# Kernel optimization log

Hardware: AMD Instinct MI355X
Metric: run time of the kernel (lower is better)

## Reference

```python
import jax, jax.numpy as jnp
import numpy as np

EPS = 1e-6
H = 16

def setup_inputs() -> dict:
    key = jax.random.key(0)
    ks = jax.random.split(key, 11)
    B, L, D = 4, 4096, 1024
    sc = 1.0 / np.sqrt(D)
    return {
        "queries": jax.random.normal(ks[0], (B, L, D), jnp.float32),
        "keys": jax.random.normal(ks[1], (B, L, D), jnp.float32),
        "values": jax.random.normal(ks[2], (B, L, D), jnp.float32),
        "Wq": jax.random.normal(ks[3], (D, D), jnp.float32) * sc,
        "bq": jax.random.normal(ks[4], (D,), jnp.float32) * 0.01,
        "Wk": jax.random.normal(ks[5], (D, D), jnp.float32) * sc,
        "bk": jax.random.normal(ks[6], (D,), jnp.float32) * 0.01,
        "Wv": jax.random.normal(ks[7], (D, D), jnp.float32) * sc,
        "bv": jax.random.normal(ks[8], (D,), jnp.float32) * 0.01,
        "Wo": jax.random.normal(ks[9], (D, D), jnp.float32) * sc,
        "bo": jax.random.normal(ks[10], (D,), jnp.float32) * 0.01,
    }

def reference(queries, keys, values, Wq, bq, Wk, bk, Wv, bv, Wo, bo):
    B, L, _ = queries.shape
    S = keys.shape[1]
    # projections + split heads: [B, H, L, dh]
    q = (queries @ Wq + bq).reshape(B, L, H, -1).transpose(0, 2, 1, 3)
    k = (keys @ Wk + bk).reshape(B, S, H, -1).transpose(0, 2, 1, 3)
    v = (values @ Wv + bv).reshape(B, S, H, -1).transpose(0, 2, 1, 3)
    # kernel feature map
    q = jax.nn.sigmoid(q)
    k = jax.nn.sigmoid(k)
    # flow normalization (sink/source)
    sink_incoming = 1.0 / jnp.einsum('nhld,nhd->nhl', q + EPS, k.sum(axis=2) + EPS)
    source_outgoing = 1.0 / jnp.einsum('nhld,nhd->nhl', k + EPS, q.sum(axis=2) + EPS)
    conserved_sink = jnp.einsum('nhld,nhd->nhl', q + EPS,
                                (k * source_outgoing[..., None]).sum(axis=2) + EPS)
    conserved_source = jnp.einsum('nhld,nhd->nhl', k + EPS,
                                  (q * sink_incoming[..., None]).sum(axis=2) + EPS)
    conserved_source = jnp.clip(conserved_source, -1.0, 1.0)
    sink_allocation = jax.nn.sigmoid(conserved_sink * (float(L) / float(S)))
    source_competition = jax.nn.softmax(conserved_source, axis=-1) * float(S)
    # linear attention: kv then q(kv)
    qn = q * sink_incoming[..., None]
    vn = v * source_competition[..., None]
    kv = jnp.einsum('nhld,nhlm->nhdm', k, vn)
    x = jnp.einsum('nhld,nhdm->nhlm', qn, kv) * sink_allocation[..., None]
    x = x.transpose(0, 2, 1, 3).reshape(B, L, -1)
    return x @ Wo + bo
```

## Files before the change

kernel.cpp:

```cpp
#include <hip/hip_runtime.h>

#define Bc 4
#define Lc 4096
#define Dc 1024
#define LDQ 3072
#define Mc (Bc*Lc)
#define EPSc 1e-6f

typedef __bf16 bf16x8 __attribute__((ext_vector_type(8)));
typedef __bf16 bf16x4 __attribute__((ext_vector_type(4)));
typedef float f32x4 __attribute__((ext_vector_type(4)));

typedef __attribute__((address_space(3))) void lds_vt;
typedef const __attribute__((address_space(1))) void gbl_vt;

__device__ __forceinline__ void gll16(const void* g, void* l) {
  __builtin_amdgcn_global_load_lds((gbl_vt*)g, (lds_vt*)l, 16, 0, 0);
}

__global__ __launch_bounds__(256) void conv3(const float* __restrict__ Q, const float* __restrict__ K,
                                             const float* __restrict__ V, __bf16* __restrict__ Y) {
  const float* src = (blockIdx.y == 0) ? Q : (blockIdx.y == 1) ? K : V;
  __bf16* dst = Y + (size_t)blockIdx.y * ((size_t)Mc * Dc);
  const int i = blockIdx.x * 256 + threadIdx.x;
  const float4 v = ((const float4*)src)[i];
  bf16x4 o;
  o[0] = (__bf16)v.x; o[1] = (__bf16)v.y; o[2] = (__bf16)v.z; o[3] = (__bf16)v.w;
  ((bf16x4*)dst)[i] = o;
}

__global__ __launch_bounds__(256) void wt_conv4(const float* __restrict__ W0, const float* __restrict__ W1,
                                                const float* __restrict__ W2, const float* __restrict__ W3,
                                                __bf16* __restrict__ T) {
  const float* W = (blockIdx.z == 0) ? W0 : (blockIdx.z == 1) ? W1 : (blockIdx.z == 2) ? W2 : W3;
  __bf16* Wt = T + (size_t)blockIdx.z * ((size_t)Dc * Dc);
  __shared__ float t[32][33];
  const int n0 = blockIdx.x << 5, k0 = blockIdx.y << 5;
  const int tx = threadIdx.x, ty = threadIdx.y;
#pragma unroll
  for (int i = 0; i < 4; ++i)
    t[ty + 8 * i][tx] = W[(size_t)(k0 + ty + 8 * i) * Dc + n0 + tx];
  __syncthreads();
#pragma unroll
  for (int i = 0; i < 4; ++i)
    Wt[(size_t)(n0 + ty + 8 * i) * Dc + k0 + tx] = (__bf16)t[tx][ty + 8 * i];
}

template <int FUSED>
__global__ __launch_bounds__(256, 4) void gemm128b(
    const __bf16* __restrict__ Aq_, const __bf16* __restrict__ Ak_, const __bf16* __restrict__ Av_,
    const __bf16* __restrict__ Wq_, const __bf16* __restrict__ Wk_, const __bf16* __restrict__ Wv_,
    const float* __restrict__ bq_, const float* __restrict__ bk_, const float* __restrict__ bv_,
    void* __restrict__ Cp, float* __restrict__ qsum, float* __restrict__ ksum) {
  __shared__ __bf16 As[2][128 * 32];
  __shared__ __bf16 Bs[2][128 * 32];
  const int tid = threadIdx.x;
  const int lane = tid & 63, w4 = tid >> 6;
  const int wr = w4 >> 1, wc = w4 & 1;
  const int lf = lane & 15, kq = lane >> 4;

  constexpr int NCT = FUSED ? 24 : 8;
  constexpr int CPX = (128 * NCT) >> 3;
  const int hwlin = blockIdx.x + (blockIdx.y << 7);
  const int swz = (hwlin & 7) * CPX + (hwlin >> 3);
  const int bx = swz / NCT, ct = swz - bx * NCT;
  const int row0 = bx << 7, col0 = ct << 7;
  const int region = FUSED ? (ct >> 3) : 0;
  const int colL = FUSED ? (col0 & 1023) : col0;

  const __bf16* Agl = FUSED ? (region == 0 ? Aq_ : (region == 1 ? Ak_ : Av_)) : Aq_;
  const __bf16* Bgl = FUSED ? (region == 0 ? Wq_ : (region == 1 ? Wk_ : Wv_)) : Wq_;
  const float* biasp = FUSED ? (region == 0 ? bq_ : (region == 1 ? bk_ : bv_)) : bq_;
  const __bf16* Ab_g = Agl + (size_t)row0 * 1024;
  const __bf16* Bb_g = Bgl + (size_t)colL * 1024;

  const int srow = (w4 << 5) + (lane >> 2);
  const int sgd = lane & 3;
  const int ssrc = (sgd ^ ((lane >> 3) & 3)) << 3;
  const size_t aoff0 = (size_t)srow * 1024 + ssrc;
  const size_t aoff1 = (size_t)(srow + 16) * 1024 + ssrc;
  const int ldst0 = srow * 32 + (sgd << 3);
  const int ldst1 = (srow + 16) * 32 + (sgd << 3);

  const int kgsw = (kq ^ ((lf >> 1) & 3)) << 3;
  const int arb = (wr * 64 + lf) * 32 + kgsw;
  const int brb = (wc * 64 + lf) * 32 + kgsw;

  f32x4 acc[4][4] = {};

  for (int t = 0; t < 16; ++t) {
    const int kb = t << 6;
    gll16(Ab_g + aoff0 + kb, &As[0][ldst0]);
    gll16(Ab_g + aoff1 + kb, &As[0][ldst1]);
    gll16(Bb_g + aoff0 + kb, &Bs[0][ldst0]);
    gll16(Bb_g + aoff1 + kb, &Bs[0][ldst1]);
    gll16(Ab_g + aoff0 + kb + 32, &As[1][ldst0]);
    gll16(Ab_g + aoff1 + kb + 32, &As[1][ldst1]);
    gll16(Bb_g + aoff0 + kb + 32, &Bs[1][ldst0]);
    gll16(Bb_g + aoff1 + kb + 32, &Bs[1][ldst1]);
    __syncthreads();
#pragma unroll
    for (int hf = 0; hf < 2; ++hf) {
      bf16x8 af[4], bfr[4];
#pragma unroll
      for (int m = 0; m < 4; ++m) af[m] = *(const bf16x8*)(&As[hf][0] + arb + m * 512);
#pragma unroll
      for (int n = 0; n < 4; ++n) bfr[n] = *(const bf16x8*)(&Bs[hf][0] + brb + n * 512);
#pragma unroll
      for (int m = 0; m < 4; ++m)
#pragma unroll
        for (int n = 0; n < 4; ++n)
          acc[m][n] = __builtin_amdgcn_mfma_f32_16x16x32_bf16(bfr[n], af[m], acc[m][n], 0, 0, 0);
    }
    __syncthreads();
  }

  const int b_of = row0 >> 12;
  const int orow = row0 + wr * 64 + lf;
  const int ocl = wc * 64 + (kq << 2);
#pragma unroll
  for (int n = 0; n < 4; ++n) {
    const int cl = ocl + (n << 4);
    const int cb = colL + cl;
    const f32x4 bb = *(const f32x4*)&biasp[cb];
    f32x4 sacc = {0.f, 0.f, 0.f, 0.f};
#pragma unroll
    for (int m = 0; m < 4; ++m) {
      f32x4 v = acc[m][n] + bb;
      if (FUSED && region < 2) {
#pragma unroll
        for (int r = 0; r < 4; ++r) v[r] = 1.0f / (1.0f + expf(-v[r]));
      }
      if (FUSED) {
        bf16x4 o;
#pragma unroll
        for (int r = 0; r < 4; ++r) o[r] = (__bf16)v[r];
        *(bf16x4*)&((__bf16*)Cp)[(size_t)(orow + (m << 4)) * LDQ + col0 + cl] = o;
      } else {
        *(f32x4*)&((float*)Cp)[(size_t)(orow + (m << 4)) * 1024 + col0 + cl] = v;
      }
      sacc += v;
    }
    if (FUSED && region < 2) {
#pragma unroll
      for (int o = 1; o < 16; o <<= 1) {
        sacc[0] += __shfl_xor(sacc[0], o); sacc[1] += __shfl_xor(sacc[1], o);
        sacc[2] += __shfl_xor(sacc[2], o); sacc[3] += __shfl_xor(sacc[3], o);
      }
      if (lf == 0) {
        float* sums = (region == 0) ? qsum : ksum;
#pragma unroll
        for (int r = 0; r < 4; ++r) atomicAdd(&sums[b_of * 1024 + cb + r], sacc[r]);
      }
    }
  }
}

template <int FUSED>
__global__ __launch_bounds__(256, 2) void gemm256x128(
    const __bf16* __restrict__ Aq_, const __bf16* __restrict__ Ak_, const __bf16* __restrict__ Av_,
    const __bf16* __restrict__ Wq_, const __bf16* __restrict__ Wk_, const __bf16* __restrict__ Wv_,
    const float* __restrict__ bq_, const float* __restrict__ bk_, const float* __restrict__ bv_,
    void* __restrict__ Cp, float* __restrict__ qsum, float* __restrict__ ksum) {
  __shared__ __bf16 As[256 * 32];
  __shared__ __bf16 Bs[128 * 32];
  const int tid = threadIdx.x;
  const int lane = tid & 63, w4 = tid >> 6;
  const int wr = w4 >> 1, wc = w4 & 1;
  const int lf = lane & 15, kq = lane >> 4;

  constexpr int NCT = FUSED ? 24 : 8;
  constexpr int CPX = (64 * NCT) >> 3;
  const int hwlin = blockIdx.x + blockIdx.y * 64;
  const int swz = (hwlin & 7) * CPX + (hwlin >> 3);
  const int bx = swz / NCT, ct = swz - bx * NCT;
  const int row0 = bx << 8, col0 = ct << 7;
  const int region = FUSED ? (ct >> 3) : 0;
  const int colL = FUSED ? (col0 & 1023) : col0;

  const __bf16* Agl = FUSED ? (region == 0 ? Aq_ : (region == 1 ? Ak_ : Av_)) : Aq_;
  const __bf16* Bgl = FUSED ? (region == 0 ? Wq_ : (region == 1 ? Wk_ : Wv_)) : Wq_;
  const float* biasp = FUSED ? (region == 0 ? bq_ : (region == 1 ? bk_ : bv_)) : bq_;
  const __bf16* Ab_g = Agl + (size_t)row0 * 1024;
  const __bf16* Bb_g = Bgl + (size_t)colL * 1024;

  int arow[4], asrc[4];
#pragma unroll
  for (int i = 0; i < 4; ++i) {
    const int g = i * 256 + tid;
    arow[i] = g >> 2;
    asrc[i] = ((g & 3) ^ ((arow[i] >> 1) & 3)) << 3;
  }
  const int kgsw = (kq ^ ((lf >> 1) & 3)) << 3;
  const int arb = (wr * 128 + lf) * 32 + kgsw;
  const int brb = (wc * 64 + lf) * 32 + kgsw;

  f32x4 acc[8][4] = {};

  for (int t = 0; t < 32; ++t) {
    const int kb = t << 5;
#pragma unroll
    for (int i = 0; i < 4; ++i)
      gll16(Ab_g + (size_t)arow[i] * 1024 + kb + asrc[i], &As[(i * 256 + tid) * 8]);
#pragma unroll
    for (int i = 0; i < 2; ++i)
      gll16(Bb_g + (size_t)arow[i] * 1024 + kb + asrc[i], &Bs[(i * 256 + tid) * 8]);
    __syncthreads();
    bf16x8 af[8], bfr[4];
#pragma unroll
    for (int m = 0; m < 8; ++m) af[m] = *(const bf16x8*)(As + arb + m * 512);
#pragma unroll
    for (int n = 0; n < 4; ++n) bfr[n] = *(const bf16x8*)(Bs + brb + n * 512);
#pragma unroll
    for (int m = 0; m < 8; ++m)
#pragma unroll
      for (int n = 0; n < 4; ++n)
        acc[m][n] = __builtin_amdgcn_mfma_f32_16x16x32_bf16(bfr[n], af[m], acc[m][n], 0, 0, 0);
    __syncthreads();
  }

  const int b_of = row0 >> 12;
  const int orow = row0 + wr * 128 + lf;
  const int ocl = wc * 64 + (kq << 2);
#pragma unroll
  for (int n = 0; n < 4; ++n) {
    const int cl = ocl + (n << 4);
    const int cb = colL + cl;
    const f32x4 bb = *(const f32x4*)&biasp[cb];
    f32x4 sacc = {0.f, 0.f, 0.f, 0.f};
#pragma unroll
    for (int m = 0; m < 8; ++m) {
      f32x4 v = acc[m][n] + bb;
      if (FUSED && region < 2) {
#pragma unroll
        for (int r = 0; r < 4; ++r) v[r] = 1.0f / (1.0f + expf(-v[r]));
      }
      if (FUSED) {
        bf16x4 o;
#pragma unroll
        for (int r = 0; r < 4; ++r) o[r] = (__bf16)v[r];
        *(bf16x4*)&((__bf16*)Cp)[(size_t)(orow + (m << 4)) * LDQ + col0 + cl] = o;
      } else {
        *(f32x4*)&((float*)Cp)[(size_t)(orow + (m << 4)) * 1024 + col0 + cl] = v;
      }
      sacc += v;
    }
    if (FUSED && region < 2) {
#pragma unroll
      for (int o = 1; o < 16; o <<= 1) {
        sacc[0] += __shfl_xor(sacc[0], o); sacc[1] += __shfl_xor(sacc[1], o);
        sacc[2] += __shfl_xor(sacc[2], o); sacc[3] += __shfl_xor(sacc[3], o);
      }
      if (lf == 0) {
        float* sums = (region == 0) ? qsum : ksum;
#pragma unroll
        for (int r = 0; r < 4; ++r) atomicAdd(&sums[b_of * 1024 + cb + r], sacc[r]);
      }
    }
  }
}

__global__ __launch_bounds__(256) void r2_flow(const __bf16* __restrict__ Qp, const __bf16* __restrict__ Kp,
                                               const float* __restrict__ ksum, const float* __restrict__ qsum,
                                               float* __restrict__ si,
                                               float* __restrict__ qsi, float* __restrict__ kso) {
  const int blk = blockIdx.x;
  const int chunk = blk & 15, bh = blk >> 4;
  const int b = bh >> 4, h = bh & 15;
  const int d = threadIdx.x & 63, w = threadIdx.x >> 6;
  __shared__ float ksE[64], qsE[64];
  if (threadIdx.x < 64) ksE[threadIdx.x] = ksum[bh * 64 + threadIdx.x] + EPSc;
  else if (threadIdx.x < 128) qsE[threadIdx.x - 64] = qsum[bh * 64 + threadIdx.x - 64] + EPSc;
  __syncthreads();
  const float kE = ksE[d], qE = qsE[d];
  const size_t base = ((size_t)b * Lc) * LDQ + h * 64 + d;
  const size_t obase = (size_t)bh * Lc;
  float qsia = 0.f, ksoa = 0.f;
  const int l0 = chunk * 256;
  for (int i = w; i < 256; i += 4) {
    const int l = l0 + i;
    const size_t idx = base + (size_t)l * LDQ;
    const float qv = (float)Qp[idx], kvv = (float)Kp[idx];
    float a = (qv + EPSc) * kE;
    float c2 = (kvv + EPSc) * qE;
#pragma unroll
    for (int o = 32; o; o >>= 1) { a += __shfl_xor(a, o); c2 += __shfl_xor(c2, o); }
    const float sil = 1.0f / a, sol = 1.0f / c2;
    if (d == 0) si[obase + l] = sil;
    qsia += qv * sil;
    ksoa += kvv * sol;
  }
  atomicAdd(&qsi[bh * 64 + d], qsia);
  atomicAdd(&kso[bh * 64 + d], ksoa);
}

__global__ __launch_bounds__(256) void r3_cons(const __bf16* __restrict__ Qp, const __bf16* __restrict__ Kp,
                                               const float* __restrict__ qsi, const float* __restrict__ kso,
                                               float* __restrict__ sa, float* __restrict__ csx,
                                               float* __restrict__ den) {
  const int blk = blockIdx.x;
  const int chunk = blk & 15, bh = blk >> 4;
  const int b = bh >> 4, h = bh & 15;
  const int d = threadIdx.x & 63, w = threadIdx.x >> 6;
  __shared__ float ksoE[64], qsiE[64];
  if (threadIdx.x < 64) ksoE[threadIdx.x] = kso[bh * 64 + threadIdx.x] + EPSc;
  else if (threadIdx.x < 128) qsiE[threadIdx.x - 64] = qsi[bh * 64 + threadIdx.x - 64] + EPSc;
  __syncthreads();
  const float kE = ksoE[d], qE = qsiE[d];
  const size_t base = ((size_t)b * Lc) * LDQ + h * 64 + d;
  const size_t obase = (size_t)bh * Lc;
  const int l0 = chunk * 256;
  float eacc = 0.f;
  for (int i = w; i < 256; i += 4) {
    const int l = l0 + i;
    const size_t idx = base + (size_t)l * LDQ;
    const float qv = (float)Qp[idx], kvv = (float)Kp[idx];
    float a = (qv + EPSc) * kE;
    float c2 = (kvv + EPSc) * qE;
#pragma unroll
    for (int o = 32; o; o >>= 1) { a += __shfl_xor(a, o); c2 += __shfl_xor(c2, o); }
    if (d == 0) {
      sa[obase + l] = 1.0f / (1.0f + expf(-a));
      const float cl = fminf(1.0f, fmaxf(-1.0f, c2));
      const float e = expf(cl);
      csx[obase + l] = e;
      eacc += e;
    }
  }
  if (d == 0) atomicAdd(&den[bh], eacc);
}

__global__ __launch_bounds__(256) void k5_kv(const __bf16* __restrict__ Kp, const __bf16* __restrict__ Vp,
                                             const float* __restrict__ csx, const float* __restrict__ den,
                                             float* __restrict__ kvout) {
  const int bh = blockIdx.x, chunk = blockIdx.y;
  const int b = bh >> 4, h = bh & 15;
  const int tid = threadIdx.x;
  const int dq = (tid >> 4) << 2;
  const int mq = (tid & 15) << 2;
  const float sden = 4096.0f / den[bh];
  __shared__ float klds[4][64], vlds[4][64];
  float acc[4][4] = {};
  const int r = tid >> 6, c = tid & 63;
  const size_t rowbase = ((size_t)b * Lc + chunk * 512) * LDQ + h * 64;
  const size_t csbase = (size_t)bh * Lc + chunk * 512;
  for (int i = 0; i < 512; i += 4) {
    const size_t idx = rowbase + (size_t)(i + r) * LDQ + c;
    const float sc = csx[csbase + i + r] * sden;
    klds[r][c] = (float)Kp[idx];
    vlds[r][c] = (float)Vp[idx] * sc;
    __syncthreads();
#pragma unroll
    for (int rr = 0; rr < 4; ++rr) {
      float kr[4], vr[4];
#pragma unroll
      for (int j = 0; j < 4; ++j) { kr[j] = klds[rr][dq + j]; vr[j] = vlds[rr][mq + j]; }
#pragma unroll
      for (int a = 0; a < 4; ++a)
#pragma unroll
        for (int e = 0; e < 4; ++e) acc[a][e] += kr[a] * vr[e];
    }
    __syncthreads();
  }
#pragma unroll
  for (int a = 0; a < 4; ++a)
#pragma unroll
    for (int e = 0; e < 4; ++e)
      atomicAdd(&kvout[(size_t)bh * 4096 + (dq + a) * 64 + mq + e], acc[a][e]);
}

__global__ __launch_bounds__(256) void k6_x(const __bf16* __restrict__ Qp,
                                            const float* __restrict__ kvin, const float* __restrict__ si,
                                            const float* __restrict__ sa, __bf16* __restrict__ Xb) {
  const int bh = blockIdx.x, chunk = blockIdx.y;
  const int b = bh >> 4, h = bh & 15;
  const int tid = threadIdx.x, lane = tid & 63, w = tid >> 6;
  const int lf = lane & 15, kq = lane >> 4;
  __shared__ float ktl[64][66];
  for (int e = tid; e < 4096; e += 256)
    ktl[e & 63][e >> 6] = kvin[(size_t)bh * 4096 + e];
  __syncthreads();
  bf16x8 kh[4][2], kl[4][2];
#pragma unroll
  for (int mi = 0; mi < 4; ++mi)
#pragma unroll
    for (int hf = 0; hf < 2; ++hf) {
      const float* p = &ktl[mi * 16 + lf][hf * 32 + kq * 8];
      bf16x8 hi, lo;
#pragma unroll
      for (int j = 0; j < 8; ++j) {
        const float f = p[j];
        hi[j] = (__bf16)f;
        lo[j] = (__bf16)(f - (float)hi[j]);
      }
      kh[mi][hf] = hi; kl[mi][hf] = lo;
    }
  const size_t bL = (size_t)b * Lc;
  const size_t obase = (size_t)bh * Lc;
#pragma unroll
  for (int gi = 0; gi < 4; ++gi) {
    const int lrow = chunk * 256 + (w * 4 + gi) * 16 + lf;
    const size_t qb = (bL + lrow) * LDQ + h * 64;
    const bf16x8 qf0 = *(const bf16x8*)(Qp + qb + kq * 8);
    const bf16x8 qf1 = *(const bf16x8*)(Qp + qb + 32 + kq * 8);
    const float sc = si[obase + lrow] * sa[obase + lrow];
    f32x4 acc[4] = {};
#pragma unroll
    for (int mi = 0; mi < 4; ++mi) {
      acc[mi] = __builtin_amdgcn_mfma_f32_16x16x32_bf16(kh[mi][0], qf0, acc[mi], 0, 0, 0);
      acc[mi] = __builtin_amdgcn_mfma_f32_16x16x32_bf16(kh[mi][1], qf1, acc[mi], 0, 0, 0);
      acc[mi] = __builtin_amdgcn_mfma_f32_16x16x32_bf16(kl[mi][0], qf0, acc[mi], 0, 0, 0);
      acc[mi] = __builtin_amdgcn_mfma_f32_16x16x32_bf16(kl[mi][1], qf1, acc[mi], 0, 0, 0);
    }
#pragma unroll
    for (int mi = 0; mi < 4; ++mi) {
      bf16x4 o;
#pragma unroll
      for (int r = 0; r < 4; ++r) o[r] = (__bf16)(acc[mi][r] * sc);
      *(bf16x4*)&Xb[(bL + lrow) * Dc + h * 64 + mi * 16 + (kq << 2)] = o;
    }
  }
}

extern "C" void kernel_launch(void* const* d_in, const int* in_sizes, int n_in,
                              void* d_out, int out_size, void* d_ws, size_t ws_size,
                              hipStream_t stream) {
  const float* Qin = (const float*)d_in[0];
  const float* Kin = (const float*)d_in[1];
  const float* Vin = (const float*)d_in[2];
  const float* Wq = (const float*)d_in[3];
  const float* bq = (const float*)d_in[4];
  const float* Wk = (const float*)d_in[5];
  const float* bk = (const float*)d_in[6];
  const float* Wv = (const float*)d_in[7];
  const float* bv = (const float*)d_in[8];
  const float* Wo = (const float*)d_in[9];
  const float* bo = (const float*)d_in[10];

  const size_t MD = (size_t)Mc * Dc;
  __bf16* Aq = (__bf16*)d_ws;
  __bf16* Ak = Aq + MD;
  __bf16* Av = Ak + MD;
  __bf16* Wqt = Av + MD;
  __bf16* Wkt = Wqt + (size_t)Dc * Dc;
  __bf16* Wvt = Wkt + (size_t)Dc * Dc;
  __bf16* Wot = Wvt + (size_t)Dc * Dc;
  __bf16* QKV = Wot + (size_t)Dc * Dc;
  float* F = (float*)(QKV + (size_t)Mc * LDQ);
  float* ksum = F;
  float* qsum = ksum + 4096;
  float* kso = qsum + 4096;
  float* qsi = kso + 4096;
  float* den = qsi + 4096;
  float* kv = den + 64;
  float* si = kv + 262144;
  float* sa = si + 262144;
  float* csx = sa + 262144;
  __bf16* Xb = Aq;

  hipMemsetAsync(F, 0, (size_t)(4 * 4096 + 64 + 262144) * sizeof(float), stream);

  conv3<<<dim3((int)(MD / 4 / 256), 3), 256, 0, stream>>>(Qin, Kin, Vin, Aq);
  wt_conv4<<<dim3(32, 32, 4), dim3(32, 8), 0, stream>>>(Wq, Wk, Wv, Wo, Wqt);

  gemm128b<1><<<dim3(128, 24), 256, 0, stream>>>(Aq, Ak, Av, Wqt, Wkt, Wvt,
                                                 bq, bk, bv, QKV, qsum, ksum);

  const __bf16* Qp = QKV;
  const __bf16* Kp = QKV + 1024;
  const __bf16* Vp = QKV + 2048;
  r2_flow<<<1024, 256, 0, stream>>>(Qp, Kp, ksum, qsum, si, qsi, kso);
  r3_cons<<<1024, 256, 0, stream>>>(Qp, Kp, qsi, kso, sa, csx, den);
  k5_kv<<<dim3(64, 8), 256, 0, stream>>>(Kp, Vp, csx, den, kv);
  k6_x<<<dim3(64, 16), 256, 0, stream>>>(Qp, kv, si, sa, Xb);

  gemm256x128<0><<<dim3(64, 8), 256, 0, stream>>>(Xb, nullptr, nullptr, Wot, nullptr, nullptr,
                                                  bo, nullptr, nullptr, d_out, nullptr, nullptr);
}
```

Measured before the change: 497.2 us.

## Fuse conserved-flow kernel into kv and x kernels, defer softmax denominator

```diff
diff --git a/kernel.cpp b/kernel.cpp
--- a/kernel.cpp
+++ b/kernel.cpp
@@ -294,61 +294,35 @@
   atomicAdd(&kso[bh * 64 + d], ksoa);
 }
 
-__global__ __launch_bounds__(256) void r3_cons(const __bf16* __restrict__ Qp, const __bf16* __restrict__ Kp,
-                                               const float* __restrict__ qsi, const float* __restrict__ kso,
-                                               float* __restrict__ sa, float* __restrict__ csx,
-                                               float* __restrict__ den) {
-  const int blk = blockIdx.x;
-  const int chunk = blk & 15, bh = blk >> 4;
-  const int b = bh >> 4, h = bh & 15;
-  const int d = threadIdx.x & 63, w = threadIdx.x >> 6;
-  __shared__ float ksoE[64], qsiE[64];
-  if (threadIdx.x < 64) ksoE[threadIdx.x] = kso[bh * 64 + threadIdx.x] + EPSc;
-  else if (threadIdx.x < 128) qsiE[threadIdx.x - 64] = qsi[bh * 64 + threadIdx.x - 64] + EPSc;
-  __syncthreads();
-  const float kE = ksoE[d], qE = qsiE[d];
-  const size_t base = ((size_t)b * Lc) * LDQ + h * 64 + d;
-  const size_t obase = (size_t)bh * Lc;
-  const int l0 = chunk * 256;
-  float eacc = 0.f;
-  for (int i = w; i < 256; i += 4) {
-    const int l = l0 + i;
-    const size_t idx = base + (size_t)l * LDQ;
-    const float qv = (float)Qp[idx], kvv = (float)Kp[idx];
-    float a = (qv + EPSc) * kE;
-    float c2 = (kvv + EPSc) * qE;
-#pragma unroll
-    for (int o = 32; o; o >>= 1) { a += __shfl_xor(a, o); c2 += __shfl_xor(c2, o); }
-    if (d == 0) {
-      sa[obase + l] = 1.0f / (1.0f + expf(-a));
-      const float cl = fminf(1.0f, fmaxf(-1.0f, c2));
-      const float e = expf(cl);
-      csx[obase + l] = e;
-      eacc += e;
-    }
-  }
-  if (d == 0) atomicAdd(&den[bh], eacc);
-}
-
 __global__ __launch_bounds__(256) void k5_kv(const __bf16* __restrict__ Kp, const __bf16* __restrict__ Vp,
-                                             const float* __restrict__ csx, const float* __restrict__ den,
+                                             const float* __restrict__ qsi, float* __restrict__ den,
                                              float* __restrict__ kvout) {
   const int bh = blockIdx.x, chunk = blockIdx.y;
   const int b = bh >> 4, h = bh & 15;
   const int tid = threadIdx.x;
   const int dq = (tid >> 4) << 2;
   const int mq = (tid & 15) << 2;
-  const float sden = 4096.0f / den[bh];
+  __shared__ float qsE[64];
   __shared__ float klds[4][64], vlds[4][64];
+  if (tid < 64) qsE[tid] = qsi[bh * 64 + tid] + EPSc;
+  __syncthreads();
   float acc[4][4] = {};
+  float eacc = 0.f;
   const int r = tid >> 6, c = tid & 63;
+  const float qE = qsE[c];
   const size_t rowbase = ((size_t)b * Lc + chunk * 512) * LDQ + h * 64;
-  const size_t csbase = (size_t)bh * Lc + chunk * 512;
   for (int i = 0; i < 512; i += 4) {
     const size_t idx = rowbase + (size_t)(i + r) * LDQ + c;
-    const float sc = csx[csbase + i + r] * sden;
-    klds[r][c] = (float)Kp[idx];
-    vlds[r][c] = (float)Vp[idx] * sc;
+    const float kvf = (float)Kp[idx];
+    const float vvf = (float)Vp[idx];
+    float c2 = (kvf + EPSc) * qE;
+#pragma unroll
+    for (int o = 32; o; o >>= 1) c2 += __shfl_xor(c2, o);
+    const float e = expf(fminf(1.0f, fmaxf(-1.0f, c2)));
+    if (c == 0) eacc += e;
+    __syncthreads();
+    klds[r][c] = kvf;
+    vlds[r][c] = vvf * e;
     __syncthreads();
 #pragma unroll
     for (int rr = 0; rr < 4; ++rr) {
@@ -358,24 +332,33 @@
 #pragma unroll
       for (int a = 0; a < 4; ++a)
 #pragma unroll
-        for (int e = 0; e < 4; ++e) acc[a][e] += kr[a] * vr[e];
-    }
-    __syncthreads();
-  }
+        for (int e2 = 0; e2 < 4; ++e2) acc[a][e2] += kr[a] * vr[e2];
+    }
+    __syncthreads();
+  }
+  if (c == 0) atomicAdd(&den[bh], eacc);
 #pragma unroll
   for (int a = 0; a < 4; ++a)
 #pragma unroll
-    for (int e = 0; e < 4; ++e)
-      atomicAdd(&kvout[(size_t)bh * 4096 + (dq + a) * 64 + mq + e], acc[a][e]);
+    for (int e2 = 0; e2 < 4; ++e2)
+      atomicAdd(&kvout[(size_t)bh * 4096 + (dq + a) * 64 + mq + e2], acc[a][e2]);
 }
 
 __global__ __launch_bounds__(256) void k6_x(const __bf16* __restrict__ Qp,
                                             const float* __restrict__ kvin, const float* __restrict__ si,
-                                            const float* __restrict__ sa, __bf16* __restrict__ Xb) {
+                                            const float* __restrict__ kso, const float* __restrict__ den,
+                                            __bf16* __restrict__ Xb) {
   const int bh = blockIdx.x, chunk = blockIdx.y;
   const int b = bh >> 4, h = bh & 15;
   const int tid = threadIdx.x, lane = tid & 63, w = tid >> 6;
   const int lf = lane & 15, kq = lane >> 4;
+  const float sden = 4096.0f / den[bh];
+  f32x4 kE0a = *(const f32x4*)&kso[bh * 64 + kq * 8];
+  f32x4 kE0b = *(const f32x4*)&kso[bh * 64 + kq * 8 + 4];
+  f32x4 kE1a = *(const f32x4*)&kso[bh * 64 + 32 + kq * 8];
+  f32x4 kE1b = *(const f32x4*)&kso[bh * 64 + 32 + kq * 8 + 4];
+#pragma unroll
+  for (int j = 0; j < 4; ++j) { kE0a[j] += EPSc; kE0b[j] += EPSc; kE1a[j] += EPSc; kE1b[j] += EPSc; }
   __shared__ float ktl[64][66];
   for (int e = tid; e < 4096; e += 256)
     ktl[e & 63][e >> 6] = kvin[(size_t)bh * 4096 + e];
@@ -403,7 +386,18 @@
     const size_t qb = (bL + lrow) * LDQ + h * 64;
     const bf16x8 qf0 = *(const bf16x8*)(Qp + qb + kq * 8);
     const bf16x8 qf1 = *(const bf16x8*)(Qp + qb + 32 + kq * 8);
-    const float sc = si[obase + lrow] * sa[obase + lrow];
+    float a = 0.f;
+#pragma unroll
+    for (int j = 0; j < 4; ++j) {
+      a += ((float)qf0[j] + EPSc) * kE0a[j];
+      a += ((float)qf0[4 + j] + EPSc) * kE0b[j];
+      a += ((float)qf1[j] + EPSc) * kE1a[j];
+      a += ((float)qf1[4 + j] + EPSc) * kE1b[j];
+    }
+    a += __shfl_xor(a, 16);
+    a += __shfl_xor(a, 32);
+    const float sav = 1.0f / (1.0f + expf(-a));
+    const float sc = si[obase + lrow] * sav * sden;
     f32x4 acc[4] = {};
 #pragma unroll
     for (int mi = 0; mi < 4; ++mi) {
@@ -454,8 +448,6 @@
   float* den = qsi + 4096;
   float* kv = den + 64;
   float* si = kv + 262144;
-  float* sa = si + 262144;
-  float* csx = sa + 262144;
   __bf16* Xb = Aq;
 
   hipMemsetAsync(F, 0, (size_t)(4 * 4096 + 64 + 262144) * sizeof(float), stream);
@@ -470,9 +462,8 @@
   const __bf16* Kp = QKV + 1024;
   const __bf16* Vp = QKV + 2048;
   r2_flow<<<1024, 256, 0, stream>>>(Qp, Kp, ksum, qsum, si, qsi, kso);
-  r3_cons<<<1024, 256, 0, stream>>>(Qp, Kp, qsi, kso, sa, csx, den);
-  k5_kv<<<dim3(64, 8), 256, 0, stream>>>(Kp, Vp, csx, den, kv);
-  k6_x<<<dim3(64, 16), 256, 0, stream>>>(Qp, kv, si, sa, Xb);
+  k5_kv<<<dim3(64, 8), 256, 0, stream>>>(Kp, Vp, qsi, den, kv);
+  k6_x<<<dim3(64, 16), 256, 0, stream>>>(Qp, kv, si, kso, den, Xb);
 
   gemm256x128<0><<<dim3(64, 8), 256, 0, stream>>>(Xb, nullptr, nullptr, Wot, nullptr, nullptr,
                                                   bo, nullptr, nullptr, d_out, nullptr, nullptr);
```

Result: faster. 461.0 us (-7.3%).
